# Kernel optimization log

Measured on AMD Instinct MI355X. Metric: run time of the kernel, lower is better.

The kernel has to match this reference:

```python
import jax, jax.numpy as jnp
import numpy as np

M, IN, OUT = 8192, 4096, 4096
BITWIDTH = 7


def psto_shift_int32(x, shift):
    """Pseudo-stochastic right-shift of int32 x by `shift` bits -> int8.
    Faithful to PstoShiftInt32: floor-divide, derive a pseudo random number
    from the low half of the remainder, compare against the high half."""
    pow_s = jnp.left_shift(jnp.int32(1), shift)
    rt = jnp.floor_divide(x, pow_s)
    prob = jnp.abs(x - rt * pow_s)
    half_pow = jnp.left_shift(jnp.int32(1), shift // 2)
    qp = jnp.floor_divide(prob, half_pow)
    prn = prob - qp * half_pow
    prn = jnp.where(shift % 2 == 1, prn * 2, prn)
    dec = jnp.where(qp <= prn, jnp.int32(0), jnp.int32(1)) * jnp.sign(x)
    return jnp.clip(rt + dec, -127, 127).astype(jnp.int8)


def range_bitwidth(x):
    # RangeEstimate: ceil(log2(max|x|)), 0 if all-zero (torch also goes via float)
    m = jnp.max(jnp.abs(x)).astype(jnp.float32)
    return jnp.where(m == 0, jnp.int32(0), jnp.ceil(jnp.log2(m)).astype(jnp.int32))


def act_calc(acc, exp_in):
    """Shift int32 accumulator back to int8 and track the block exponent."""
    bw = range_bitwidth(acc)
    shift = bw - BITWIDTH
    # shift>1 -> shift by `shift`; shift==1 -> shift by 2; else -> plain int8 cast
    eff = jnp.where(shift > 1, shift, jnp.where(shift == 1, jnp.int32(2), jnp.int32(0)))
    rounded = psto_shift_int32(acc, jnp.maximum(eff, 0))
    out = jnp.where(eff > 0, rounded, acc.astype(jnp.int8))  # int8 cast wraps, as in torch
    exp_out = (exp_in + eff).astype(jnp.int8)
    return out, exp_out


def setup_inputs() -> dict:
    key = jax.random.key(0)
    k1, k2 = jax.random.split(key)
    # int8-valued tensors kept in int32 containers for the matmul accumulate
    act_in = jax.random.randint(k1, (M, IN), -127, 128, dtype=jnp.int32)
    weight = jax.random.randint(k2, (OUT, IN), -127, 128, dtype=jnp.int32)
    return {"act_in": act_in, "exp_in": -6, "weight": weight, "weight_exp": -9}


def reference(act_in, exp_in, weight, weight_exp):
    # the roundoff4 padding in the original is a no-op)
    acc = jnp.matmul(act_in, weight.T)  # [M, OUT] int32
    act_out, exp_out = act_calc(acc, jnp.int32(exp_in) + jnp.int32(weight_exp))
    return act_out, exp_out
```

## Files before the change

kernel.cpp:

```cpp
#include <hip/hip_runtime.h>
#include <stdint.h>
#include <math.h>

#define M_DIM 8192
#define N_DIM 4096
#define K_DIM 4096
#define BITWIDTH 7

#define BM 128
#define BN 128
#define BK 128

using i32x4  = __attribute__((ext_vector_type(4)))  int;
using i32x16 = __attribute__((ext_vector_type(16))) int;

__global__ __launch_bounds__(256) void pack_both_kernel(
        const int* __restrict__ act, const int* __restrict__ wt,
        uint32_t* __restrict__ act8, uint32_t* __restrict__ w8,
        int* __restrict__ maxabs) {
    if (blockIdx.x == 0 && threadIdx.x == 0) *maxabs = 0;
    const int ACT_N8 = (M_DIM * K_DIM) / 8;
    int i = blockIdx.x * blockDim.x + threadIdx.x;
    const int* src;
    uint32_t* dst;
    if (i < ACT_N8) { src = act; dst = act8; }
    else            { src = wt;  dst = w8;  i -= ACT_N8; }
    int4 a = ((const int4*)src)[2 * i];
    int4 b = ((const int4*)src)[2 * i + 1];
    uint32_t p0 = (uint32_t)(a.x & 0xFF) | ((uint32_t)(a.y & 0xFF) << 8)
                | ((uint32_t)(a.z & 0xFF) << 16) | ((uint32_t)(a.w & 0xFF) << 24);
    uint32_t p1 = (uint32_t)(b.x & 0xFF) | ((uint32_t)(b.y & 0xFF) << 8)
                | ((uint32_t)(b.z & 0xFF) << 16) | ((uint32_t)(b.w & 0xFF) << 24);
    ((uint2*)dst)[i] = make_uint2(p0, p1);
}

__device__ __forceinline__ void gload_lds16(const int8_t* g, int8_t* lds) {
    __builtin_amdgcn_global_load_lds(
        (__attribute__((address_space(1))) void*)g,
        (__attribute__((address_space(3))) void*)lds,
        16, 0, 0);
}

__global__ __launch_bounds__(256) void gemm_i8(const int8_t* __restrict__ A8,
                                               const int8_t* __restrict__ B8,
                                               int* __restrict__ C,
                                               int* __restrict__ maxabs) {
    __shared__ __align__(16) int8_t As[BM * BK];
    __shared__ __align__(16) int8_t Bs[BN * BK];
    __shared__ int wmaxs[4];

    const int tid  = threadIdx.x;
    const int wave = tid >> 6;
    const int lane = tid & 63;

    const int row0 = blockIdx.y * BM;
    const int col0 = blockIdx.x * BN;

    const int wm = (wave >> 1) * 64;
    const int wn = (wave & 1) * 64;

    i32x16 acc[2][2];
#pragma unroll
    for (int i = 0; i < 2; ++i)
#pragma unroll
        for (int j = 0; j < 2; ++j)
            acc[i][j] = (i32x16)(0);

    const int ra     = wave * 32;
    const int rowoff = lane >> 3;
    const int chk    = ((lane & 7) ^ rowoff) << 4;

    const int8_t* ag = A8 + (size_t)(row0 + ra + rowoff) * K_DIM + chk;
    const int8_t* bg = B8 + (size_t)(col0 + ra + rowoff) * K_DIM + chk;

    const int fr  = lane & 31;
    const int hl  = lane >> 5;
    const int swz = fr & 7;
    int aoff[2][4], boff[2][4];
#pragma unroll
    for (int kk = 0; kk < 4; ++kk) {
        int c = kk * 2 + hl;
        int co = ((c ^ swz) << 4);
#pragma unroll
        for (int i = 0; i < 2; ++i) {
            aoff[i][kk] = (wm + i * 32 + fr) * BK + co;
            boff[i][kk] = (wn + i * 32 + fr) * BK + co;
        }
    }

    for (int k0 = 0; k0 < K_DIM; k0 += BK) {
        __syncthreads();
#pragma unroll
        for (int g = 0; g < 4; ++g) {
            gload_lds16(ag + k0 + (size_t)(8 * g) * K_DIM, As + (ra + 8 * g) * BK);
            gload_lds16(bg + k0 + (size_t)(8 * g) * K_DIM, Bs + (ra + 8 * g) * BK);
        }
        __syncthreads();

#pragma unroll
        for (int kk = 0; kk < 4; ++kk) {
            i32x4 af[2], bf[2];
#pragma unroll
            for (int i = 0; i < 2; ++i) {
                af[i] = *(const i32x4*)(As + aoff[i][kk]);
                bf[i] = *(const i32x4*)(Bs + boff[i][kk]);
            }
#pragma unroll
            for (int i = 0; i < 2; ++i)
#pragma unroll
                for (int j = 0; j < 2; ++j)
                    acc[i][j] = __builtin_amdgcn_mfma_i32_32x32x32_i8(
                        af[i], bf[j], acc[i][j], 0, 0, 0);
        }
    }

    int mymax = 0;
    const int ccol = lane & 31;
    const int rbase = hl << 2;
#pragma unroll
    for (int i = 0; i < 2; ++i) {
#pragma unroll
        for (int j = 0; j < 2; ++j) {
            int* p = C + (size_t)(row0 + wm + i * 32) * N_DIM
                       + (col0 + wn + j * 32 + ccol);
#pragma unroll
            for (int r = 0; r < 16; ++r) {
                int row = (r & 3) + 8 * (r >> 2) + rbase;
                int v = acc[i][j][r];
                p[(size_t)row * N_DIM] = v;
                int a = v < 0 ? -v : v;
                mymax = a > mymax ? a : mymax;
            }
        }
    }

#pragma unroll
    for (int off = 32; off > 0; off >>= 1) {
        int o = __shfl_down(mymax, off, 64);
        mymax = o > mymax ? o : mymax;
    }
    if (lane == 0) wmaxs[wave] = mymax;
    __syncthreads();
    if (tid == 0) {
        int bmx = wmaxs[0];
        for (int w = 1; w < 4; ++w) bmx = wmaxs[w] > bmx ? wmaxs[w] : bmx;
        atomicMax(maxabs, bmx);
    }
}

__device__ __forceinline__ int psto(int x, int eff) {
    if (eff > 0) {
        int rt   = x >> eff;
        int prob = x & ((1 << eff) - 1);
        int h    = eff >> 1;
        int qp   = prob >> h;
        int prn  = (prob & ((1 << h) - 1)) << (eff & 1);
        int sgn  = (x > 0) - (x < 0);
        int r    = rt + ((qp <= prn) ? 0 : sgn);
        r = r < -127 ? -127 : r;
        r = r > 127 ? 127 : r;
        return r;
    }
    return (int)(int8_t)x;
}

__global__ __launch_bounds__(256) void finalize_kernel(int* __restrict__ C,
        const int* __restrict__ maxabs,
        const int* __restrict__ exp_in,
        const int* __restrict__ wexp) {
    const int m = *maxabs;
    int bw = 0;
    if (m != 0) bw = (int)ceilf(log2f((float)m));
    const int shift = bw - BITWIDTH;
    const int eff = (shift > 1) ? shift : ((shift == 1) ? 2 : 0);

    const size_t idx = ((size_t)blockIdx.x * blockDim.x + threadIdx.x) * 8;
    int4 v0 = *(const int4*)(C + idx);
    int4 v1 = *(const int4*)(C + idx + 4);
    int4 o0, o1;
    o0.x = psto(v0.x, eff); o0.y = psto(v0.y, eff);
    o0.z = psto(v0.z, eff); o0.w = psto(v0.w, eff);
    o1.x = psto(v1.x, eff); o1.y = psto(v1.y, eff);
    o1.z = psto(v1.z, eff); o1.w = psto(v1.w, eff);
    *(int4*)(C + idx) = o0;
    *(int4*)(C + idx + 4) = o1;

    if (idx == 0) {
        C[(size_t)M_DIM * N_DIM] = (int)(int8_t)(exp_in[0] + wexp[0] + eff);
    }
}

extern "C" void kernel_launch(void* const* d_in, const int* in_sizes, int n_in,
                              void* d_out, int out_size, void* d_ws, size_t ws_size,
                              hipStream_t stream) {
    const int* act    = (const int*)d_in[0];
    const int* exp_in = (const int*)d_in[1];
    const int* wt     = (const int*)d_in[2];
    const int* wexp   = (const int*)d_in[3];

    int8_t* act8   = (int8_t*)d_ws;
    int8_t* w8     = act8 + (size_t)M_DIM * K_DIM;
    int*    maxabs = (int*)(w8 + (size_t)N_DIM * K_DIM);

    pack_both_kernel<<<24576, 256, 0, stream>>>(
        act, wt, (uint32_t*)act8, (uint32_t*)w8, maxabs);

    int* C = (int*)d_out;
    dim3 grid(N_DIM / BN, M_DIM / BM);
    gemm_i8<<<grid, 256, 0, stream>>>(act8, w8, C, maxabs);

    finalize_kernel<<<((size_t)M_DIM * N_DIM / 8) / 256, 256, 0, stream>>>(
        C, maxabs, exp_in, wexp);
}
```

Before: 448.5 us.

## Double-buffer LDS tiles in int8 GEMM to overlap global loads with MFMA

Splits the GEMM shared-memory tiles into two buffers. The next K-slice is issued with direct global-to-LDS loads while MFMAs run on the current buffer, so there is one barrier per slice instead of two. It also sets a launch bound of two blocks per CU. This hides global load latency behind compute, at the cost of doubling LDS per block (64KB), which may reduce occupancy.

```diff
diff --git a/kernel.cpp b/kernel.cpp
--- a/kernel.cpp
+++ b/kernel.cpp
@@ -41,12 +41,11 @@
         16, 0, 0);
 }
 
-__global__ __launch_bounds__(256) void gemm_i8(const int8_t* __restrict__ A8,
-                                               const int8_t* __restrict__ B8,
-                                               int* __restrict__ C,
-                                               int* __restrict__ maxabs) {
-    __shared__ __align__(16) int8_t As[BM * BK];
-    __shared__ __align__(16) int8_t Bs[BN * BK];
+__global__ __launch_bounds__(256, 2) void gemm_i8(
+        const int8_t* __restrict__ A8, const int8_t* __restrict__ B8,
+        int* __restrict__ C, int* __restrict__ maxabs) {
+    __shared__ __align__(16) int8_t As[2][BM * BK];
+    __shared__ __align__(16) int8_t Bs[2][BN * BK];
     __shared__ int wmaxs[4];
 
     const int tid  = threadIdx.x;
@@ -79,8 +78,7 @@
     int aoff[2][4], boff[2][4];
 #pragma unroll
     for (int kk = 0; kk < 4; ++kk) {
-        int c = kk * 2 + hl;
-        int co = ((c ^ swz) << 4);
+        int co = (((kk * 2 + hl) ^ swz) << 4);
 #pragma unroll
         for (int i = 0; i < 2; ++i) {
             aoff[i][kk] = (wm + i * 32 + fr) * BK + co;
@@ -88,22 +86,23 @@
         }
     }
 
-    for (int k0 = 0; k0 < K_DIM; k0 += BK) {
-        __syncthreads();
+    auto issue = [&](int k0, int buf) {
 #pragma unroll
         for (int g = 0; g < 4; ++g) {
-            gload_lds16(ag + k0 + (size_t)(8 * g) * K_DIM, As + (ra + 8 * g) * BK);
-            gload_lds16(bg + k0 + (size_t)(8 * g) * K_DIM, Bs + (ra + 8 * g) * BK);
-        }
-        __syncthreads();
-
+            gload_lds16(ag + k0 + (size_t)(8 * g) * K_DIM,
+                        As[buf] + (ra + 8 * g) * BK);
+            gload_lds16(bg + k0 + (size_t)(8 * g) * K_DIM,
+                        Bs[buf] + (ra + 8 * g) * BK);
+        }
+    };
+    auto compute = [&](int buf) {
 #pragma unroll
         for (int kk = 0; kk < 4; ++kk) {
             i32x4 af[2], bf[2];
 #pragma unroll
             for (int i = 0; i < 2; ++i) {
-                af[i] = *(const i32x4*)(As + aoff[i][kk]);
-                bf[i] = *(const i32x4*)(Bs + boff[i][kk]);
+                af[i] = *(const i32x4*)(As[buf] + aoff[i][kk]);
+                bf[i] = *(const i32x4*)(Bs[buf] + boff[i][kk]);
             }
 #pragma unroll
             for (int i = 0; i < 2; ++i)
@@ -112,6 +111,16 @@
                     acc[i][j] = __builtin_amdgcn_mfma_i32_32x32x32_i8(
                         af[i], bf[j], acc[i][j], 0, 0, 0);
         }
+    };
+
+    issue(0, 0);
+    for (int k0 = 0; k0 < K_DIM; k0 += 2 * BK) {
+        __syncthreads();
+        if (k0 + BK < K_DIM) issue(k0 + BK, 1);
+        compute(0);
+        __syncthreads();
+        if (k0 + 2 * BK < K_DIM) issue(k0 + 2 * BK, 0);
+        if (k0 + BK < K_DIM) compute(1);
     }
 
     int mymax = 0;
```

New measurement: 463.2 us. 3.3% more time.
